# Optimization experiments

Measured on AMD Instinct MI355X. Metric: run time of the kernel, lower is better.

Reference implementation:

```python
import jax, jax.numpy as jnp
import numpy as np

N = 16_777_216
H, W = 239, 319            # shape=(320,240): H=shape[1]-1, W=shape[0]-1
TIME_DIV = 4               # group_num=8 // 2
PSH, PSW = 16, 16          # patch_size
PH, PW = (H + 1) // PSH, (W + 1) // PSW   # 15, 20
TOKEN_NUM = PH * PW        # 300
PATCH_SIZE = PSH * PSW     # 256
B = 1e-4
TOTAL = TIME_DIV * 2 * PATCH_SIZE * TOKEN_NUM  # index[0]*bins[0]


def setup_inputs() -> dict:
    key = jax.random.key(0)
    k1, k2, k3, k4 = jax.random.split(key, 4)
    # events: (t sorted ascending, x in [0,W), y in [0,H), polarity in {0,1})
    t = jnp.sort(jax.random.uniform(k1, (N,), minval=0.0, maxval=1e4))
    xs = jax.random.uniform(k2, (N,), minval=0.0, maxval=float(W))
    ys = jax.random.uniform(k3, (N,), minval=0.0, maxval=float(H))
    p = jax.random.randint(k4, (N,), 0, 2).astype(jnp.float32)
    x = jnp.stack([t, xs, ys, p], axis=1)  # [N, 4], no inf values
    return {"x": x}


def reference(x):
    # x: [N, 4] columns (t, x, y, polarity); assumed inf-free (torch filter is a no-op)
    w = (x[:, 3] != 2).astype(x.dtype)                       # polarity-valid weight
    t = x[:, 0]
    wt = (t - t[0]) / (t[-1] - t[0] + B)                     # normalized-time weight
    pos = (jnp.floor(x[:, 1] / (W / PW + B))
           + jnp.floor(x[:, 2] / (H / PH + B)) * PW)         # which patch
    tok = (jnp.floor(x[:, 1] % (W / PW + B))
           + jnp.floor(x[:, 2] % (H / PH + B)) * ((W + 1) // PW))  # within-patch index
    dtime = jnp.floor(TIME_DIV * (t - t[0]) / (t[-1] - t[0] + 1.0))
    # multi-index -> 1-D (index_mapping): clamp each dim to [0, bins[d]] then ravel
    bins = jnp.array([TIME_DIV, 2, PATCH_SIZE, TOKEN_NUM], dtype=jnp.int32)
    index = jnp.array([2 * PATCH_SIZE * TOKEN_NUM, PATCH_SIZE * TOKEN_NUM,
                       TOKEN_NUM, 1], dtype=jnp.int32)
    x_nd = jnp.stack([dtime, x[:, 3], tok, pos]).astype(jnp.int32)  # [4, N]
    y_cl = jnp.clip(x_nd, 0, bins[:, None])
    l = jnp.sum(index[:, None] * y_cl, axis=0)                # [N] flat indices
    # two weighted histograms sharing the same indices (torch.bincount x2)
    h_w = jax.ops.segment_sum(w, l, num_segments=TOTAL).reshape(TIME_DIV, 2, PATCH_SIZE, TOKEN_NUM)
    h_wt = jax.ops.segment_sum(wt, l, num_segments=TOTAL).reshape(TIME_DIV, 2, PATCH_SIZE, TOKEN_NUM)
    y = jnp.stack([h_w, h_wt], axis=2)                        # [T, 2, 2, Patch, Token]
    return y.reshape(1, -1, PH, PW)
```

## Files before the change

### kernel.cpp

```cpp
#include <hip/hip_runtime.h>
#include <stdint.h>


#define TPB 512
#define B1 4096
#define CHUNK 4096
#define EVT (CHUNK / TPB)
#define NBUCKET 2400
#define SCAN_PER 5
#define GACC 16
#define NG (NBUCKET / GACC)
#define SLICES 8
#define RPS (B1 / SLICES)
#define HCELLS (GACC * 256)
#define ATPB 512
#define OUT_CH_STRIDE 76800
#define OUT_DP_STRIDE 153600

__device__ __forceinline__ void classify_full(const float4 e, const float t0,
                                              const float d_wt, const float d_dt,
                                              int& bucket, int& tok, float& wt) {
    const float c1 = (float)(319.0 / 20.0 + 1e-4);
    const float c2 = (float)(239.0 / 15.0 + 1e-4);
    const int pos = (int)(floorf(e.y / c1) + floorf(e.z / c2) * 20.0f);
    tok = (int)(floorf(fmodf(e.y, c1)) + floorf(fmodf(e.z, c2)) * 16.0f);
    const int dt = (int)floorf(4.0f * (e.x - t0) / d_dt);
    const int p  = (int)e.w;
    bucket = (dt * 2 + p) * 300 + pos;
    wt = (e.x - t0) / d_wt;
}

__global__ __launch_bounds__(TPB) void k_bin(const float4* __restrict__ x,
                                             uint32_t* __restrict__ payload,
                                             uint16_t* __restrict__ pfxT,
                                             int n) {
    __shared__ uint32_t stage[CHUNK];
    __shared__ uint32_t cnt[NBUCKET];
    __shared__ uint32_t wsum[TPB / 64];

    for (int i = threadIdx.x; i < NBUCKET; i += TPB) cnt[i] = 0;
    __syncthreads();

    const float* xf = (const float*)x;
    const float t0 = xf[0];
    const float tlast = xf[(size_t)(n - 1) * 4];
    const float d_wt = tlast - t0 + 1e-4f;
    const float d_dt = tlast - t0 + 1.0f;

    const int beg = blockIdx.x * CHUNK;
    const bool full = (beg + CHUNK <= n);

    uint32_t pk[EVT];
    uint32_t bk[EVT];
    if (full) {
        #pragma unroll
        for (int k = 0; k < EVT; ++k) {
            float4 e = x[beg + threadIdx.x + k * TPB];
            int bucket, tok; float wt;
            classify_full(e, t0, d_wt, d_dt, bucket, tok, wt);
            uint32_t q = (uint32_t)(wt * 1048576.0f);
            q = q > 1048575u ? 1048575u : q;
            pk[k] = ((uint32_t)tok << 24) | ((uint32_t)(bucket & 15) << 20) | q;
            uint32_t rank = atomicAdd(&cnt[bucket], 1u);
            bk[k] = (uint32_t)bucket | (rank << 12);
        }
    } else {
        #pragma unroll
        for (int k = 0; k < EVT; ++k) {
            const int i = beg + threadIdx.x + k * TPB;
            if (i < n) {
                float4 e = x[i];
                int bucket, tok; float wt;
                classify_full(e, t0, d_wt, d_dt, bucket, tok, wt);
                uint32_t q = (uint32_t)(wt * 1048576.0f);
                q = q > 1048575u ? 1048575u : q;
                pk[k] = ((uint32_t)tok << 24) | ((uint32_t)(bucket & 15) << 20) | q;
                uint32_t rank = atomicAdd(&cnt[bucket], 1u);
                bk[k] = (uint32_t)bucket | (rank << 12);
            } else {
                bk[k] = 0xFFFFFFFFu;
            }
        }
    }
    __syncthreads();

    uint32_t v[SCAN_PER];
    uint32_t sum = 0;
    const int base_i = threadIdx.x * SCAN_PER;
    #pragma unroll
    for (int j = 0; j < SCAN_PER; ++j) {
        int idx = base_i + j;
        uint32_t c = (idx < NBUCKET) ? cnt[idx] : 0u;
        v[j] = sum;
        sum += c;
    }
    uint32_t inc = sum;
    #pragma unroll
    for (int off = 1; off < 64; off <<= 1) {
        uint32_t u = __shfl_up(inc, off, 64);
        if ((threadIdx.x & 63) >= off) inc += u;
    }
    const int wid = threadIdx.x >> 6, lid = threadIdx.x & 63;
    if (lid == 63) wsum[wid] = inc;
    __syncthreads();
    uint32_t woff = 0;
    for (int w = 0; w < wid; ++w) woff += wsum[w];
    const uint32_t excl = woff + inc - sum;

    #pragma unroll
    for (int j = 0; j < SCAN_PER; ++j) {
        int idx = base_i + j;
        if (idx < NBUCKET) {
            uint32_t p = excl + v[j];
            cnt[idx] = p;
            if ((idx & 15) == 0)
                pfxT[(size_t)(idx >> 4) * B1 + blockIdx.x] = (uint16_t)p;
        }
    }
    __syncthreads();

    if (full) {
        #pragma unroll
        for (int k = 0; k < EVT; ++k)
            stage[cnt[bk[k] & 0xFFFu] + (bk[k] >> 12)] = pk[k];
    } else {
        #pragma unroll
        for (int k = 0; k < EVT; ++k)
            if (bk[k] != 0xFFFFFFFFu)
                stage[cnt[bk[k] & 0xFFFu] + (bk[k] >> 12)] = pk[k];
    }
    __syncthreads();

    const int end = min(beg + CHUNK, n);
    const int cntE = end > beg ? end - beg : 0;
    uint32_t* pbase = payload + (size_t)blockIdx.x * CHUNK;
    const int n4 = cntE >> 2;
    const uint4* s4 = (const uint4*)stage;
    uint4* g4 = (uint4*)pbase;
    for (int i = threadIdx.x; i < n4; i += TPB) g4[i] = s4[i];
    for (int i = (n4 << 2) + threadIdx.x; i < cntE; i += TPB) pbase[i] = stage[i];
}

__global__ __launch_bounds__(ATPB) void k_accum(const uint32_t* __restrict__ payload,
                                                const uint16_t* __restrict__ pfxT,
                                                unsigned long long* __restrict__ partial,
                                                int n) {
    const int g = blockIdx.x >> 3;
    const int s = blockIdx.x & 7;

    __shared__ unsigned long long hist[HCELLS];
    for (int i = threadIdx.x; i < HCELLS; i += ATPB) hist[i] = 0ULL;
    __syncthreads();

    const uint16_t* colb = pfxT + (size_t)g * B1;
    const bool last = (g == NG - 1);
    const uint16_t* cole = colb + B1;

    const int wid = threadIdx.x >> 6, lid = threadIdx.x & 63;
    const int r0 = s * RPS + wid * 64;

    const int row = r0 + lid;
    uint32_t vb = colb[row];
    uint32_t ve;
    if (!last) {
        ve = cole[row];
    } else {
        int rc = n - row * CHUNK;
        ve = rc < 0 ? 0 : (rc > CHUNK ? CHUNK : rc);
    }

    const int q4 = lid >> 4;
    const int ql = lid & 15;
    for (int r = 0; r < 64; r += 4) {
        const int rr = r + q4;
        const uint32_t sb = __shfl(vb, rr, 64);
        const uint32_t se = __shfl(ve, rr, 64);
        const uint32_t* seg = payload + (size_t)(r0 + rr) * CHUNK;
        for (uint32_t j = sb + ql; j < se; j += 16) {
            const uint32_t w = seg[j];
            atomicAdd(&hist[w >> 20],
                      (1ULL << 40) | (unsigned long long)(w & 0xFFFFFu));
        }
    }
    __syncthreads();

    unsigned long long* pp = partial + ((size_t)s * NG + g) * HCELLS;
    for (int i = threadIdx.x; i < HCELLS; i += ATPB) pp[i] = hist[i];
}

__global__ __launch_bounds__(256) void k_out(const unsigned long long* __restrict__ partial,
                                             float* __restrict__ out) {
    const int i = blockIdx.x * 256 + threadIdx.x;
    unsigned long long v = 0ULL;
    #pragma unroll
    for (int s = 0; s < SLICES; ++s)
        v += partial[(size_t)s * (NG * HCELLS) + i];
    const int g = i >> 12;
    const int idx = i & 4095;
    const int tok = idx >> 4;
    const int c = idx & 15;
    const int b = g * GACC + c;
    const int pos = b % 300;
    const int dp = b / 300;
    const float cntf = (float)(uint32_t)(v >> 40);
    const float wts  = (float)(v & ((1ULL << 40) - 1)) * (1.0f / 1048576.0f);
    const int base0 = dp * OUT_DP_STRIDE + tok * 300 + pos;
    out[base0] = cntf;
    out[base0 + OUT_CH_STRIDE] = wts;
}

__global__ __launch_bounds__(256) void e2src_hist_atomic(const float4* __restrict__ x,
                                                         float* __restrict__ out, int n) {
    const float* xf = (const float*)x;
    const float t0 = xf[0];
    const float tlast = xf[(size_t)(n - 1) * 4];
    const float d_wt = tlast - t0 + 1e-4f;
    const float d_dt = tlast - t0 + 1.0f;
    int i = blockIdx.x * blockDim.x + threadIdx.x;
    const int stride = gridDim.x * blockDim.x;
    for (; i < n; i += stride) {
        float4 e = x[i];
        int bucket, tok; float wt;
        classify_full(e, t0, d_wt, d_dt, bucket, tok, wt);
        const int dp = bucket / 300, pos = bucket % 300;
        const int base = dp * OUT_DP_STRIDE + tok * 300 + pos;
        unsafeAtomicAdd(out + base, 1.0f);
        unsafeAtomicAdd(out + base + OUT_CH_STRIDE, wt);
    }
}

extern "C" void kernel_launch(void* const* d_in, const int* in_sizes, int n_in,
                              void* d_out, int out_size, void* d_ws, size_t ws_size,
                              hipStream_t stream) {
    const float* x = (const float*)d_in[0];
    float* out = (float*)d_out;
    const int n = in_sizes[0] / 4;

    const size_t payload_bytes = ((size_t)n * 4u + 7u) & ~(size_t)7u;
    const size_t pfx_bytes = (size_t)B1 * NG * 2u;
    const size_t part_bytes = (size_t)SLICES * NG * HCELLS * 8u;
    const size_t need = payload_bytes + pfx_bytes + part_bytes;

    if (ws_size < need || n > B1 * CHUNK || n <= 0) {
        hipMemsetAsync(d_out, 0, (size_t)out_size * sizeof(float), stream);
        if (n > 0)
            hipLaunchKernelGGL(e2src_hist_atomic, dim3(8192), dim3(256), 0, stream,
                               (const float4*)x, out, n);
        return;
    }

    uint32_t* payload = (uint32_t*)d_ws;
    uint16_t* pfxT = (uint16_t*)((char*)d_ws + payload_bytes);
    unsigned long long* partial =
        (unsigned long long*)((char*)d_ws + payload_bytes + pfx_bytes);

    hipLaunchKernelGGL(k_bin, dim3(B1), dim3(TPB), 0, stream,
                       (const float4*)x, payload, pfxT, n);
    hipLaunchKernelGGL(k_accum, dim3(NG * SLICES), dim3(ATPB), 0, stream,
                       payload, pfxT, partial, n);
    hipLaunchKernelGGL(k_out, dim3((NG * HCELLS) / 256), dim3(256), 0, stream,
                       partial, out);
}
```

Baseline: 449.1 us.

## Bin events by 16-bucket group with smaller chunks and interleaved slices

The binning kernel now counts and scatters by bucket group (150 groups) rather than the full 2400 buckets. That shrinks the shared counter array and replaces the 5-per-thread scan with one value per thread. Chunk size is halved and threads per block are halved, giving twice as many blocks. The accumulation kernel assigns rows to slices in an interleaved pattern, so each slice covers the whole time range, and fmodf is replaced with an explicit floor-and-subtract remainder. Within a group, events are no longer sorted by exact bucket, and the explicit remainder may differ from fmodf rounding in edge cases.

```diff
diff --git a/kernel.cpp b/kernel.cpp
--- a/kernel.cpp
+++ b/kernel.cpp
@@ -2,16 +2,16 @@
 #include <stdint.h>
 
 
-#define TPB 512
-#define B1 4096
-#define CHUNK 4096
+#define TPB 256
+#define B1 8192
+#define CHUNK 2048
 #define EVT (CHUNK / TPB)
 #define NBUCKET 2400
-#define SCAN_PER 5
 #define GACC 16
 #define NG (NBUCKET / GACC)
 #define SLICES 8
 #define RPS (B1 / SLICES)
+#define RPW (RPS / 8)
 #define HCELLS (GACC * 256)
 #define ATPB 512
 #define OUT_CH_STRIDE 76800
@@ -22,8 +22,12 @@
                                               int& bucket, int& tok, float& wt) {
     const float c1 = (float)(319.0 / 20.0 + 1e-4);
     const float c2 = (float)(239.0 / 15.0 + 1e-4);
-    const int pos = (int)(floorf(e.y / c1) + floorf(e.z / c2) * 20.0f);
-    tok = (int)(floorf(fmodf(e.y, c1)) + floorf(fmodf(e.z, c2)) * 16.0f);
+    const float fy = floorf(e.y / c1);
+    const float fz = floorf(e.z / c2);
+    const float remy = e.y - fy * c1;
+    const float remz = e.z - fz * c2;
+    const int pos = (int)(fy + fz * 20.0f);
+    tok = (int)(floorf(remy) + floorf(remz) * 16.0f);
     const int dt = (int)floorf(4.0f * (e.x - t0) / d_dt);
     const int p  = (int)e.w;
     bucket = (dt * 2 + p) * 300 + pos;
@@ -35,10 +39,10 @@
                                              uint16_t* __restrict__ pfxT,
                                              int n) {
     __shared__ uint32_t stage[CHUNK];
-    __shared__ uint32_t cnt[NBUCKET];
+    __shared__ uint32_t cnt[NG];
     __shared__ uint32_t wsum[TPB / 64];
 
-    for (int i = threadIdx.x; i < NBUCKET; i += TPB) cnt[i] = 0;
+    if (threadIdx.x < NG) cnt[threadIdx.x] = 0;
     __syncthreads();
 
     const float* xf = (const float*)x;
@@ -61,8 +65,9 @@
             uint32_t q = (uint32_t)(wt * 1048576.0f);
             q = q > 1048575u ? 1048575u : q;
             pk[k] = ((uint32_t)tok << 24) | ((uint32_t)(bucket & 15) << 20) | q;
-            uint32_t rank = atomicAdd(&cnt[bucket], 1u);
-            bk[k] = (uint32_t)bucket | (rank << 12);
+            const int g = bucket >> 4;
+            uint32_t rank = atomicAdd(&cnt[g], 1u);
+            bk[k] = (uint32_t)g | (rank << 8);
         }
     } else {
         #pragma unroll
@@ -75,8 +80,9 @@
                 uint32_t q = (uint32_t)(wt * 1048576.0f);
                 q = q > 1048575u ? 1048575u : q;
                 pk[k] = ((uint32_t)tok << 24) | ((uint32_t)(bucket & 15) << 20) | q;
-                uint32_t rank = atomicAdd(&cnt[bucket], 1u);
-                bk[k] = (uint32_t)bucket | (rank << 12);
+                const int g = bucket >> 4;
+                uint32_t rank = atomicAdd(&cnt[g], 1u);
+                bk[k] = (uint32_t)g | (rank << 8);
             } else {
                 bk[k] = 0xFFFFFFFFu;
             }
@@ -84,17 +90,8 @@
     }
     __syncthreads();
 
-    uint32_t v[SCAN_PER];
-    uint32_t sum = 0;
-    const int base_i = threadIdx.x * SCAN_PER;
-    #pragma unroll
-    for (int j = 0; j < SCAN_PER; ++j) {
-        int idx = base_i + j;
-        uint32_t c = (idx < NBUCKET) ? cnt[idx] : 0u;
-        v[j] = sum;
-        sum += c;
-    }
-    uint32_t inc = sum;
+    const uint32_t c = (threadIdx.x < NG) ? cnt[threadIdx.x] : 0u;
+    uint32_t inc = c;
     #pragma unroll
     for (int off = 1; off < 64; off <<= 1) {
         uint32_t u = __shfl_up(inc, off, 64);
@@ -105,29 +102,23 @@
     __syncthreads();
     uint32_t woff = 0;
     for (int w = 0; w < wid; ++w) woff += wsum[w];
-    const uint32_t excl = woff + inc - sum;
-
-    #pragma unroll
-    for (int j = 0; j < SCAN_PER; ++j) {
-        int idx = base_i + j;
-        if (idx < NBUCKET) {
-            uint32_t p = excl + v[j];
-            cnt[idx] = p;
-            if ((idx & 15) == 0)
-                pfxT[(size_t)(idx >> 4) * B1 + blockIdx.x] = (uint16_t)p;
-        }
+    const uint32_t excl = woff + inc - c;
+
+    if (threadIdx.x < NG) {
+        cnt[threadIdx.x] = excl;
+        pfxT[(size_t)threadIdx.x * B1 + blockIdx.x] = (uint16_t)excl;
     }
     __syncthreads();
 
     if (full) {
         #pragma unroll
         for (int k = 0; k < EVT; ++k)
-            stage[cnt[bk[k] & 0xFFFu] + (bk[k] >> 12)] = pk[k];
+            stage[cnt[bk[k] & 0xFFu] + (bk[k] >> 8)] = pk[k];
     } else {
         #pragma unroll
         for (int k = 0; k < EVT; ++k)
             if (bk[k] != 0xFFFFFFFFu)
-                stage[cnt[bk[k] & 0xFFFu] + (bk[k] >> 12)] = pk[k];
+                stage[cnt[bk[k] & 0xFFu] + (bk[k] >> 8)] = pk[k];
     }
     __syncthreads();
 
@@ -157,29 +148,30 @@
     const uint16_t* cole = colb + B1;
 
     const int wid = threadIdx.x >> 6, lid = threadIdx.x & 63;
-    const int r0 = s * RPS + wid * 64;
-
-    const int row = r0 + lid;
-    uint32_t vb = colb[row];
-    uint32_t ve;
-    if (!last) {
-        ve = cole[row];
-    } else {
-        int rc = n - row * CHUNK;
-        ve = rc < 0 ? 0 : (rc > CHUNK ? CHUNK : rc);
-    }
-
+    const int s0 = wid * RPW;
     const int q4 = lid >> 4;
     const int ql = lid & 15;
-    for (int r = 0; r < 64; r += 4) {
-        const int rr = r + q4;
-        const uint32_t sb = __shfl(vb, rr, 64);
-        const uint32_t se = __shfl(ve, rr, 64);
-        const uint32_t* seg = payload + (size_t)(r0 + rr) * CHUNK;
-        for (uint32_t j = sb + ql; j < se; j += 16) {
-            const uint32_t w = seg[j];
-            atomicAdd(&hist[w >> 20],
-                      (1ULL << 40) | (unsigned long long)(w & 0xFFFFFu));
+
+    for (int h = 0; h < RPW; h += 64) {
+        const int row = (s0 + h + lid) * SLICES + s;
+        uint32_t vb = colb[row];
+        uint32_t ve;
+        if (!last) {
+            ve = cole[row];
+        } else {
+            int rc = n - row * CHUNK;
+            ve = rc < 0 ? 0 : (rc > CHUNK ? CHUNK : rc);
+        }
+        for (int r = 0; r < 64; r += 4) {
+            const int rr = r + q4;
+            const uint32_t sb = __shfl(vb, rr, 64);
+            const uint32_t se = __shfl(ve, rr, 64);
+            const uint32_t* seg = payload + (size_t)((s0 + h + rr) * SLICES + s) * CHUNK;
+            for (uint32_t j = sb + ql; j < se; j += 16) {
+                const uint32_t w = seg[j];
+                atomicAdd(&hist[w >> 20],
+                          (1ULL << 40) | (unsigned long long)(w & 0xFFFFFu));
+            }
         }
     }
     __syncthreads();
```

After: 454.1 us. No clear change (+1.1%).
